# Performance work log

Hardware: AMD Instinct MI355X
Metric: run time of the kernel (lower is better)

## Reference

```python
import jax, jax.numpy as jnp
import numpy as np

B, N_DET, N_T, NY, NX = 4, 128, 2048, 256, 256


def setup_inputs() -> dict:
    key = jax.random.key(0)
    k1, k2, k3 = jax.random.split(key, 3)
    sino = jax.random.normal(k1, (B, 1, N_DET, N_T), dtype=jnp.float32)
    # LUT channel 0: floor temporal index (stored as float, cast to int in forward)
    k_floor = jax.random.randint(k2, (NY, NX, N_DET), 0, N_T).astype(jnp.float32)
    # LUT channel 1: linear interpolation weight alpha in [0,1)
    alpha = jax.random.uniform(k3, (NY, NX, N_DET), dtype=jnp.float32)
    lut = jnp.stack([k_floor, alpha], axis=-1)  # [NY, NX, N_DET, 2]
    return {"sino": sino, "lut": lut}


def reference(sino, lut):
    # sino: [B, 1, n_det, n_t]; lut: [ny, nx, n_det, 2]
    b, c, n_det, n_t = sino.shape
    k_floor = lut[..., 0].astype(jnp.int32)          # [ny, nx, n_det]
    alpha = lut[..., 1]                               # [ny, nx, n_det]
    valid = (k_floor >= 0) & (k_floor < n_t - 1)
    k0 = jnp.clip(k_floor, 0, n_t - 2)
    k1 = k0 + 1
    S = sino[:, 0]                                    # [B, n_det, n_t]
    det = jnp.arange(n_det)                           # broadcasts against [ny,nx,n_det]
    s0 = S[:, det, k0]                                # [B, ny, nx, n_det]
    s1 = S[:, det, k1]                                # [B, ny, nx, n_det]
    sk = (1.0 - alpha) * s0 + alpha * s1
    sk = jnp.where(valid, sk, jnp.zeros_like(sk))
    # Hann apodization window over detectors
    apod = (0.5 - 0.5 * jnp.cos(2.0 * jnp.pi * jnp.arange(n_det, dtype=jnp.float32)
                                / max(n_det - 1, 1))).astype(sino.dtype)
    out = jnp.einsum('bijd,d->bij', sk, apod)
    norm = jnp.maximum(apod.sum(), 1e-06)
    out = out / norm
    return out[:, None]                               # [B, 1, ny, nx]
```

## Files before the change

### kernel.cpp

```cpp
#include <hip/hip_runtime.h>
#include <hip/hip_fp16.h>


#define NB      4
#define NDET    128
#define NT      2048
#define NPIX    65536
#define PXW     8

typedef unsigned uv4 __attribute__((ext_vector_type(4)));

__global__ __launch_bounds__(256)
void cvt16b(const float* __restrict__ sino, uint4* __restrict__ ws) {
    const int id = blockIdx.x * 256 + threadIdx.x;
    const int t  = id & (NT - 1);
    float c0 = sino[id];
    float c1 = sino[id +     NDET * NT];
    float c2 = sino[id + 2 * NDET * NT];
    float c3 = sino[id + 3 * NDET * NT];
    const int idn = (t < NT - 1) ? id + 1 : id;
    float n0 = sino[idn];
    float n1 = sino[idn +     NDET * NT];
    float n2 = sino[idn + 2 * NDET * NT];
    float n3 = sino[idn + 3 * NDET * NT];
    uint4 u;
    __half2 h;
    h = __floats2half2_rn(c0, c1); u.x = *(unsigned*)&h;
    h = __floats2half2_rn(c2, c3); u.y = *(unsigned*)&h;
    h = __floats2half2_rn(n0, n1); u.z = *(unsigned*)&h;
    h = __floats2half2_rn(n2, n3); u.w = *(unsigned*)&h;
    ws[id] = u;
}

__device__ __forceinline__ float wave_reduce_add(float v) {
    int x;
    x = __builtin_amdgcn_update_dpp(0, __float_as_int(v), 0xB1,  0xF, 0xF, true); v += __int_as_float(x);
    x = __builtin_amdgcn_update_dpp(0, __float_as_int(v), 0x4E,  0xF, 0xF, true); v += __int_as_float(x);
    x = __builtin_amdgcn_update_dpp(0, __float_as_int(v), 0x141, 0xF, 0xF, true); v += __int_as_float(x);
    x = __builtin_amdgcn_update_dpp(0, __float_as_int(v), 0x140, 0xF, 0xF, true); v += __int_as_float(x);
    x = __builtin_amdgcn_update_dpp(0, __float_as_int(v), 0x142, 0xF, 0xF, true); v += __int_as_float(x);
    x = __builtin_amdgcn_update_dpp(0, __float_as_int(v), 0x143, 0xF, 0xF, true); v += __int_as_float(x);
    return v;
}

__device__ __forceinline__ void lerp_acc(unsigned kbits, unsigned abits,
                                         const uint4* __restrict__ row,
                                         float apod_d, float acc[NB]) {
    int k = (int)__uint_as_float(kbits);
    bool valid = (unsigned)k < (unsigned)(NT - 1);
    int k0 = valid ? k : 0;
    uint4 e = row[k0];
    float af = __uint_as_float(abits);
    __half2 a01 = *(__half2*)&e.x, a23 = *(__half2*)&e.y;
    __half2 b01 = *(__half2*)&e.z, b23 = *(__half2*)&e.w;
    __half2 a2  = __float2half2_rn(af);
    __half2 s01 = __hfma2(a2, __hsub2(b01, a01), a01);
    __half2 s23 = __hfma2(a2, __hsub2(b23, a23), a23);
    float w = valid ? apod_d : 0.0f;
    float2 f01 = __half22float2(s01);
    float2 f23 = __half22float2(s23);
    acc[0] = fmaf(w, f01.x, acc[0]);
    acc[1] = fmaf(w, f01.y, acc[1]);
    acc[2] = fmaf(w, f23.x, acc[2]);
    acc[3] = fmaf(w, f23.y, acc[3]);
}

__global__ __launch_bounds__(256, 4)
void bp_det(const uint4* __restrict__ ws,
            const float* __restrict__ lut,
            float* __restrict__ out) {
    const int tid  = threadIdx.x;
    const int lane = tid & 63;
    const int wid  = (blockIdx.x << 2) + (tid >> 6);
    const int px0  = wid * PXW;

    const int d0 = 2 * lane, d1 = 2 * lane + 1;
    const float C = 6.28318530717958647692f / 127.0f;
    const float apod0 = 0.5f - 0.5f * __cosf((float)d0 * C);
    const float apod1 = 0.5f - 0.5f * __cosf((float)d1 * C);

    const uint4* row0 = ws + (size_t)d0 * NT;
    const uint4* row1 = ws + (size_t)d1 * NT;
    const uv4*  lut4  = (const uv4*)lut;

    float res[NB] = {0.f, 0.f, 0.f, 0.f};

#pragma unroll
    for (int j = 0; j < PXW; ++j) {
        const int px = px0 + j;
        uv4 l = __builtin_nontemporal_load(lut4 + ((size_t)px * 64 + lane));
        float acc[NB] = {0.f, 0.f, 0.f, 0.f};
        lerp_acc(l.x, l.y, row0, apod0, acc);
        lerp_acc(l.z, l.w, row1, apod1, acc);
#pragma unroll
        for (int b = 0; b < NB; ++b) {
            float t = wave_reduce_add(acc[b]);
            float t63 = __shfl(t, 63, 64);
            res[b] = (lane == j) ? t63 : res[b];
        }
    }

    const float inv_norm = 1.0f / 63.5f;
    if (lane < PXW) {
#pragma unroll
        for (int b = 0; b < NB; ++b)
            out[(size_t)b * NPIX + px0 + lane] = res[b] * inv_norm;
    }
}

#define DBLOCK  8
#define DQ      4
#define PTILE   2048
#define THREADS 1024
#define PXPT    (PTILE / THREADS)

__global__ __launch_bounds__(256)
void cvt_kernel(const float* __restrict__ sino, uint2* __restrict__ ws16) {
    const int id = blockIdx.x * 256 + threadIdx.x;
    float v0 = sino[id];
    float v1 = sino[id + NDET * NT];
    float v2 = sino[id + 2 * NDET * NT];
    float v3 = sino[id + 3 * NDET * NT];
    __half2 h01 = __floats2half2_rn(v0, v1);
    __half2 h23 = __floats2half2_rn(v2, v3);
    uint2 u;
    u.x = *(const unsigned*)&h01;
    u.y = *(const unsigned*)&h23;
    ws16[id] = u;
}

__global__ __launch_bounds__(THREADS, 4)
void bp_kernel(const uint2* __restrict__ ws16,
               const float* __restrict__ lut,
               float* __restrict__ out) {
    __shared__ uint2 lds2[DQ * NT];

    const int tid   = threadIdx.x;
    const int octet = blockIdx.x & 15;
    const int tile  = blockIdx.x >> 4;
    const int d0    = octet * DBLOCK;
    const int px0   = tile * PTILE;

    float apod[DBLOCK];
#pragma unroll
    for (int j = 0; j < DBLOCK; ++j) {
        float x = (float)(d0 + j) * (6.28318530717958647692f / 127.0f);
        apod[j] = 0.5f - 0.5f * __cosf(x);
    }

    float acc[PXPT][NB];
#pragma unroll
    for (int i = 0; i < PXPT; ++i)
#pragma unroll
        for (int b = 0; b < NB; ++b) acc[i][b] = 0.0f;

    const float4* lp[PXPT];
#pragma unroll
    for (int i = 0; i < PXPT; ++i)
        lp[i] = (const float4*)
            (lut + ((size_t)(px0 + tid + i * THREADS) * NDET + d0) * 2);

    float4 Lcur[PXPT][2];
#pragma unroll
    for (int i = 0; i < PXPT; ++i) {
        Lcur[i][0] = lp[i][0];
        Lcur[i][1] = lp[i][1];
    }

    {
        const uint4* src = (const uint4*)(ws16 + (size_t)d0 * NT);
        uint4* dst = (uint4*)lds2;
#pragma unroll
        for (int r = 0; r < 4; ++r) dst[tid + r * THREADS] = src[tid + r * THREADS];
    }
    __syncthreads();

    float4 Lnext[PXPT][2];
#pragma unroll
    for (int i = 0; i < PXPT; ++i) {
        Lnext[i][0] = lp[i][2];
        Lnext[i][1] = lp[i][3];
    }

    auto gather = [&](const float4 (*Lq)[2], int jbase) {
#pragma unroll
        for (int i = 0; i < PXPT; ++i) {
#pragma unroll
            for (int q = 0; q < 2; ++q) {
                float4 Le = Lq[i][q];
#pragma unroll
                for (int h = 0; h < 2; ++h) {
                    float kf = h ? Le.z : Le.x;
                    float af = h ? Le.w : Le.y;
                    int   dl = q * 2 + h;
                    int k = (int)kf;
                    bool valid = (unsigned)k < (unsigned)(NT - 1);
                    float w  = valid ? apod[jbase + dl] : 0.0f;
                    int  k0  = valid ? k : 0;
                    uint2 e0 = lds2[dl * NT + k0];
                    uint2 e1 = lds2[dl * NT + k0 + 1];
                    __half2 a01 = *(__half2*)&e0.x, a23 = *(__half2*)&e0.y;
                    __half2 b01 = *(__half2*)&e1.x, b23 = *(__half2*)&e1.y;
                    __half2 a2  = __float2half2_rn(af);
                    __half2 s01 = __hfma2(a2, __hsub2(b01, a01), a01);
                    __half2 s23 = __hfma2(a2, __hsub2(b23, a23), a23);
                    float2 f01 = __half22float2(s01);
                    float2 f23 = __half22float2(s23);
                    acc[i][0] = fmaf(w, f01.x, acc[i][0]);
                    acc[i][1] = fmaf(w, f01.y, acc[i][1]);
                    acc[i][2] = fmaf(w, f23.x, acc[i][2]);
                    acc[i][3] = fmaf(w, f23.y, acc[i][3]);
                }
            }
        }
    };

    gather(Lcur, 0);
    __syncthreads();

    {
        const uint4* src = (const uint4*)(ws16 + (size_t)(d0 + DQ) * NT);
        uint4* dst = (uint4*)lds2;
#pragma unroll
        for (int r = 0; r < 4; ++r) dst[tid + r * THREADS] = src[tid + r * THREADS];
    }
    __syncthreads();

    gather(Lnext, DQ);

    const float inv_norm = 1.0f / 63.5f;
#pragma unroll
    for (int i = 0; i < PXPT; ++i) {
        const int px = px0 + tid + i * THREADS;
#pragma unroll
        for (int b = 0; b < NB; ++b) {
            atomicAdd(&out[(size_t)b * NPIX + px], acc[i][b] * inv_norm);
        }
    }
}

__global__ __launch_bounds__(512, 4)
void bp_fallback(const float* __restrict__ sino,
                 const float* __restrict__ lut,
                 float* __restrict__ out) {
    __shared__ __half2 lds[4][NT];
    const int tid   = threadIdx.x;
    const int octet = blockIdx.x & 15;
    const int tile  = blockIdx.x >> 4;
    const int d0    = octet * DBLOCK;
    const int px0   = tile * 1024;
    float apod[DBLOCK];
#pragma unroll
    for (int j = 0; j < DBLOCK; ++j) {
        float x = (float)(d0 + j) * (6.28318530717958647692f / 127.0f);
        apod[j] = 0.5f - 0.5f * __cosf(x);
    }
    float4 L[2][4];
#pragma unroll
    for (int i = 0; i < 2; ++i) {
        const float4* lq = (const float4*)
            (lut + ((size_t)(px0 + tid + i * 512) * NDET + d0) * 2);
#pragma unroll
        for (int q = 0; q < 4; ++q) L[i][q] = lq[q];
    }
    float acc[2][NB];
#pragma unroll
    for (int i = 0; i < 2; ++i)
#pragma unroll
        for (int b = 0; b < NB; ++b) acc[i][b] = 0.0f;
    const float4* s4 = (const float4*)sino;
    for (int ph = 0; ph < 4; ++ph) {
        const int b0  = (ph >> 1) * 2;
        const int dh  = ph & 1;
        const int dg0 = d0 + dh * 4;
        if (ph) __syncthreads();
        for (int f = tid; f < 4 * (NT / 4); f += 512) {
            int dl = f >> 9;
            int t4 = f & 511;
            size_t row = ((size_t)b0 * NDET + dg0 + dl) * (NT / 4) + t4;
            float4 ve = s4[row];
            float4 vo = s4[row + (size_t)NDET * (NT / 4)];
            __half2* dstp = &lds[dl][t4 * 4];
            dstp[0] = __floats2half2_rn(ve.x, vo.x);
            dstp[1] = __floats2half2_rn(ve.y, vo.y);
            dstp[2] = __floats2half2_rn(ve.z, vo.z);
            dstp[3] = __floats2half2_rn(ve.w, vo.w);
        }
        __syncthreads();
#pragma unroll
        for (int i = 0; i < 2; ++i) {
#pragma unroll
            for (int q2 = 0; q2 < 2; ++q2) {
                float4 Lq = L[i][dh * 2 + q2];
#pragma unroll
                for (int h = 0; h < 2; ++h) {
                    float kf = h ? Lq.z : Lq.x;
                    float af = h ? Lq.w : Lq.y;
                    int   dl = q2 * 2 + h;
                    int k = (int)kf;
                    bool valid = (unsigned)k < (unsigned)(NT - 1);
                    float w  = valid ? apod[dh * 4 + dl] : 0.0f;
                    int  k0  = valid ? k : 0;
                    __half2 s0v = lds[dl][k0];
                    __half2 s1v = lds[dl][k0 + 1];
                    __half2 a2  = __float2half2_rn(af);
                    __half2 sk  = __hfma2(a2, __hsub2(s1v, s0v), s0v);
                    float2  fv  = __half22float2(sk);
                    acc[i][b0 + 0] = fmaf(w, fv.x, acc[i][b0 + 0]);
                    acc[i][b0 + 1] = fmaf(w, fv.y, acc[i][b0 + 1]);
                }
            }
        }
    }
    const float inv_norm = 1.0f / 63.5f;
#pragma unroll
    for (int i = 0; i < 2; ++i) {
        const int px = px0 + tid + i * 512;
#pragma unroll
        for (int b = 0; b < NB; ++b)
            atomicAdd(&out[(size_t)b * NPIX + px], acc[i][b] * inv_norm);
    }
}

extern "C" void kernel_launch(void* const* d_in, const int* in_sizes, int n_in,
                              void* d_out, int out_size, void* d_ws, size_t ws_size,
                              hipStream_t stream) {
    const float* sino = (const float*)d_in[0];
    const float* lut  = (const float*)d_in[1];
    float* out = (float*)d_out;

    const size_t ws_new = (size_t)NDET * NT * sizeof(uint4);
    const size_t ws_old = (size_t)NDET * NT * sizeof(uint2);

    if (ws_size >= ws_new) {
        uint4* ws = (uint4*)d_ws;
        cvt16b<<<dim3(NDET * NT / 256), dim3(256), 0, stream>>>(sino, ws);
        bp_det<<<dim3(NPIX / PXW / 4), dim3(256), 0, stream>>>(ws, lut, out);
    } else if (ws_size >= ws_old) {
        (void)hipMemsetAsync(d_out, 0, (size_t)out_size * sizeof(float), stream);
        uint2* ws16 = (uint2*)d_ws;
        cvt_kernel<<<dim3(NDET * NT / 256), dim3(256), 0, stream>>>(sino, ws16);
        bp_kernel<<<dim3(512), dim3(THREADS), 0, stream>>>(ws16, lut, out);
    } else {
        (void)hipMemsetAsync(d_out, 0, (size_t)out_size * sizeof(float), stream);
        bp_fallback<<<dim3(1024), dim3(512), 0, stream>>>(sino, lut, out);
    }
}
```

Before: 144.7 us.

## Stream LUT through LDS with async global_load_lds pipeline, 16 pixels per wave

```diff
diff --git a/kernel.cpp b/kernel.cpp
--- a/kernel.cpp
+++ b/kernel.cpp
@@ -6,9 +6,11 @@
 #define NDET    128
 #define NT      2048
 #define NPIX    65536
-#define PXW     8
-
-typedef unsigned uv4 __attribute__((ext_vector_type(4)));
+#define NPXW    16
+#define DEPTH   4
+
+typedef __attribute__((address_space(3))) void lds_void;
+typedef const __attribute__((address_space(1))) void gbl_void;
 
 __global__ __launch_bounds__(256)
 void cvt16b(const float* __restrict__ sino, uint4* __restrict__ ws) {
@@ -43,65 +45,120 @@
     return v;
 }
 
-__device__ __forceinline__ void lerp_acc(unsigned kbits, unsigned abits,
-                                         const uint4* __restrict__ row,
-                                         float apod_d, float acc[NB]) {
-    int k = (int)__uint_as_float(kbits);
-    bool valid = (unsigned)k < (unsigned)(NT - 1);
-    int k0 = valid ? k : 0;
-    uint4 e = row[k0];
-    float af = __uint_as_float(abits);
-    __half2 a01 = *(__half2*)&e.x, a23 = *(__half2*)&e.y;
-    __half2 b01 = *(__half2*)&e.z, b23 = *(__half2*)&e.w;
-    __half2 a2  = __float2half2_rn(af);
-    __half2 s01 = __hfma2(a2, __hsub2(b01, a01), a01);
-    __half2 s23 = __hfma2(a2, __hsub2(b23, a23), a23);
-    float w = valid ? apod_d : 0.0f;
-    float2 f01 = __half22float2(s01);
-    float2 f23 = __half22float2(s23);
-    acc[0] = fmaf(w, f01.x, acc[0]);
-    acc[1] = fmaf(w, f01.y, acc[1]);
-    acc[2] = fmaf(w, f23.x, acc[2]);
-    acc[3] = fmaf(w, f23.y, acc[3]);
-}
-
 __global__ __launch_bounds__(256, 4)
 void bp_det(const uint4* __restrict__ ws,
             const float* __restrict__ lut,
             float* __restrict__ out) {
+    __shared__ uint4 lbuf[4][DEPTH][64];
+
     const int tid  = threadIdx.x;
     const int lane = tid & 63;
-    const int wid  = (blockIdx.x << 2) + (tid >> 6);
-    const int px0  = wid * PXW;
-
-    const int d0 = 2 * lane, d1 = 2 * lane + 1;
+    const int wv   = tid >> 6;
+    const int wid  = (blockIdx.x << 2) + wv;
+    const int px0  = wid * NPXW;
+
+    const int da = 2 * lane, db = 2 * lane + 1;
     const float C = 6.28318530717958647692f / 127.0f;
-    const float apod0 = 0.5f - 0.5f * __cosf((float)d0 * C);
-    const float apod1 = 0.5f - 0.5f * __cosf((float)d1 * C);
-
-    const uint4* row0 = ws + (size_t)d0 * NT;
-    const uint4* row1 = ws + (size_t)d1 * NT;
-    const uv4*  lut4  = (const uv4*)lut;
+    const float apodA = 0.5f - 0.5f * __cosf((float)da * C);
+    const float apodB = 0.5f - 0.5f * __cosf((float)db * C);
+
+    const uint4* rowA = ws + (size_t)da * NT;
+    const uint4* rowB = ws + (size_t)db * NT;
+
+    const float* lsrc = lut + (size_t)px0 * (NDET * 2) + lane * 4;
+
+    auto DMA = [&](int p) {
+        __builtin_amdgcn_global_load_lds(
+            (gbl_void*)(lsrc + (size_t)p * (NDET * 2)),
+            (lds_void*)&lbuf[wv][p & (DEPTH - 1)][0],
+            16, 0, 0);
+    };
+
+    float acc[NPXW][NB];
+#pragma unroll
+    for (int p = 0; p < NPXW; ++p)
+#pragma unroll
+        for (int b = 0; b < NB; ++b) acc[p][b] = 0.0f;
+
+    uint4 cA, cB;
+    float cwA, cwB;
+    unsigned caA, caB;
+
+    auto DECODE = [&](uint4 e) {
+        int k0 = (int)__uint_as_float(e.x);
+        int k1 = (int)__uint_as_float(e.z);
+        bool v0 = (unsigned)k0 < (unsigned)(NT - 1);
+        bool v1 = (unsigned)k1 < (unsigned)(NT - 1);
+        cwA = v0 ? apodA : 0.0f;
+        cwB = v1 ? apodB : 0.0f;
+        __half2 h;
+        h = __float2half2_rn(__uint_as_float(e.y)); caA = *(unsigned*)&h;
+        h = __float2half2_rn(__uint_as_float(e.w)); caB = *(unsigned*)&h;
+        cA = rowA[v0 ? k0 : 0];
+        cB = rowB[v1 ? k1 : 0];
+    };
+
+    auto LERP = [&](float (&a4)[NB]) {
+        {
+            uint4 e = cA;
+            __half2 a01 = *(__half2*)&e.x, a23 = *(__half2*)&e.y;
+            __half2 b01 = *(__half2*)&e.z, b23 = *(__half2*)&e.w;
+            __half2 a2  = *(__half2*)&caA;
+            __half2 s01 = __hfma2(a2, __hsub2(b01, a01), a01);
+            __half2 s23 = __hfma2(a2, __hsub2(b23, a23), a23);
+            float2 f01 = __half22float2(s01), f23 = __half22float2(s23);
+            a4[0] = fmaf(cwA, f01.x, a4[0]);
+            a4[1] = fmaf(cwA, f01.y, a4[1]);
+            a4[2] = fmaf(cwA, f23.x, a4[2]);
+            a4[3] = fmaf(cwA, f23.y, a4[3]);
+        }
+        {
+            uint4 e = cB;
+            __half2 a01 = *(__half2*)&e.x, a23 = *(__half2*)&e.y;
+            __half2 b01 = *(__half2*)&e.z, b23 = *(__half2*)&e.w;
+            __half2 a2  = *(__half2*)&caB;
+            __half2 s01 = __hfma2(a2, __hsub2(b01, a01), a01);
+            __half2 s23 = __hfma2(a2, __hsub2(b23, a23), a23);
+            float2 f01 = __half22float2(s01), f23 = __half22float2(s23);
+            a4[0] = fmaf(cwB, f01.x, a4[0]);
+            a4[1] = fmaf(cwB, f01.y, a4[1]);
+            a4[2] = fmaf(cwB, f23.x, a4[2]);
+            a4[3] = fmaf(cwB, f23.y, a4[3]);
+        }
+    };
+
+    DMA(0); DMA(1); DMA(2);
+    asm volatile("s_waitcnt vmcnt(2)" ::: "memory");
+    __builtin_amdgcn_sched_barrier(0);
+    DECODE(lbuf[wv][0][lane]);
+    DMA(3);
+
+#pragma unroll
+    for (int p = 0; p < NPXW; ++p) {
+        if (p + 4 < NPXW) {
+            asm volatile("s_waitcnt vmcnt(1)" ::: "memory");
+        } else {
+            asm volatile("s_waitcnt vmcnt(0)" ::: "memory");
+        }
+        __builtin_amdgcn_sched_barrier(0);
+        LERP(acc[p]);
+        if (p + 1 < NPXW) DECODE(lbuf[wv][(p + 1) & (DEPTH - 1)][lane]);
+        if (p + 4 < NPXW) DMA(p + 4);
+    }
 
     float res[NB] = {0.f, 0.f, 0.f, 0.f};
-
-#pragma unroll
-    for (int j = 0; j < PXW; ++j) {
-        const int px = px0 + j;
-        uv4 l = __builtin_nontemporal_load(lut4 + ((size_t)px * 64 + lane));
-        float acc[NB] = {0.f, 0.f, 0.f, 0.f};
-        lerp_acc(l.x, l.y, row0, apod0, acc);
-        lerp_acc(l.z, l.w, row1, apod1, acc);
+#pragma unroll
+    for (int j = 0; j < NPXW; ++j) {
 #pragma unroll
         for (int b = 0; b < NB; ++b) {
-            float t = wave_reduce_add(acc[b]);
+            float t = wave_reduce_add(acc[j][b]);
             float t63 = __shfl(t, 63, 64);
             res[b] = (lane == j) ? t63 : res[b];
         }
     }
 
     const float inv_norm = 1.0f / 63.5f;
-    if (lane < PXW) {
+    if (lane < NPXW) {
 #pragma unroll
         for (int b = 0; b < NB; ++b)
             out[(size_t)b * NPIX + px0 + lane] = res[b] * inv_norm;
@@ -335,7 +392,7 @@
     if (ws_size >= ws_new) {
         uint4* ws = (uint4*)d_ws;
         cvt16b<<<dim3(NDET * NT / 256), dim3(256), 0, stream>>>(sino, ws);
-        bp_det<<<dim3(NPIX / PXW / 4), dim3(256), 0, stream>>>(ws, lut, out);
+        bp_det<<<dim3(NPIX / NPXW / 4), dim3(256), 0, stream>>>(ws, lut, out);
     } else if (ws_size >= ws_old) {
         (void)hipMemsetAsync(d_out, 0, (size_t)out_size * sizeof(float), stream);
         uint2* ws16 = (uint2*)d_ws;
```

After: 135.0 us. 1.07x faster.
